# Optimization experiments

Measured on AMD Instinct MI355X. Metric: run time of the kernel, lower is better.

## Reference

```python
import jax, jax.numpy as jnp
import numpy as np

B, T, E, H = 4, 4096, 1024, 64

def setup_inputs() -> dict:
    key = jax.random.key(0)
    kx, kk, kq, kv = jax.random.split(key, 4)
    return {
        "x": jax.random.normal(kx, (B, T, E), dtype=jnp.float32),
        "Wk": jax.random.normal(kk, (E, H), dtype=jnp.float32) * (E ** -0.5),
        "Wq": jax.random.normal(kq, (E, H), dtype=jnp.float32) * (E ** -0.5),
        "Wv": jax.random.normal(kv, (E, H), dtype=jnp.float32) * (E ** -0.5),
    }

def reference(x, Wk, Wq, Wv):
    # x: [B, T, E]; projections: [B, T, H]
    k = jnp.einsum("bte,eh->bth", x, Wk)
    q = jnp.einsum("bte,eh->bth", x, Wq)
    v = jnp.einsum("bte,eh->bth", x, Wv)
    # NOTE: original scales by embedding dim (x.shape[-1]), not head dim.
    scale = x.shape[-1] ** -0.5
    scores = jnp.einsum("bqh,bkh->bqk", q, k) * scale  # [B, T, T]
    t = x.shape[1]
    causal = jnp.tril(jnp.ones((t, t), dtype=bool))
    scores = jnp.where(causal[None, :, :], scores, -jnp.inf)
    attn = jax.nn.softmax(scores, axis=-1)
    # dropout_rate = 0 (eval) -> identity
    return jnp.einsum("bqk,bkh->bqh", attn, v)
```

## Files before the change

kernel.cpp:

```cpp
#include <hip/hip_runtime.h>
#include <hip/hip_bf16.h>

typedef __attribute__((ext_vector_type(8))) short s16x8;
typedef __attribute__((ext_vector_type(4))) float f32x4;

#define TSEQ 4096
#define SPLIT 8

static __device__ __forceinline__ ushort f2bf(float f) {
    union { float f; unsigned u; } v; v.f = f;
    unsigned u = v.u;
    unsigned r = (u + 0x7fffu + ((u >> 16) & 1u)) >> 16;
    return (ushort)r;
}

static __device__ __forceinline__ s16x8 mk8(unsigned a, unsigned b, unsigned c, unsigned d) {
    union { uint4 u; s16x8 v; } x; x.u = make_uint4(a, b, c, d); return x.v;
}

static __device__ __forceinline__ void gload_lds16(const void* g, void* l) {
    __builtin_amdgcn_global_load_lds(
        (const __attribute__((address_space(1))) unsigned int*)g,
        (__attribute__((address_space(3))) unsigned int*)l, 16, 0, 0);
}

__global__ __launch_bounds__(256) void prep_w(const float* __restrict__ Wk,
                                              const float* __restrict__ Wq,
                                              const float* __restrict__ Wv,
                                              ushort* __restrict__ wt) {
    __shared__ float tile[64][65];
    int bid = blockIdx.x;
    int mi = bid >> 4;
    int e0 = (bid & 15) << 6;
    const float* src = (mi == 0) ? Wq : (mi == 1) ? Wk : Wv;
    int n = threadIdx.x & 63;
    int quad = threadIdx.x >> 6;
#pragma unroll
    for (int r = 0; r < 16; ++r) {
        int el = r * 4 + quad;
        tile[el][n] = src[(size_t)(e0 + el) * 64 + n];
    }
    __syncthreads();
    float scale = (mi == 0) ? 0.03125f : 1.0f;
    int ecol = threadIdx.x & 63;
#pragma unroll
    for (int r = 0; r < 16; ++r) {
        int nl = r * 4 + quad;
        wt[(size_t)(mi * 64 + nl) * 1024 + e0 + ecol] = f2bf(tile[ecol][nl] * scale);
    }
}

__global__ __launch_bounds__(512) void proj(const float* __restrict__ x,
                                            const ushort* __restrict__ wt,
                                            ushort* __restrict__ qb,
                                            ushort* __restrict__ kb,
                                            ushort* __restrict__ vt) {
    __shared__ char smem[3 * 40960];
    int tid = threadIdx.x;
    int lane = tid & 63, w = tid >> 6;
    int l15 = lane & 15, g = lane >> 4;
    int mh = w >> 2, nq = w & 3;
    size_t m0 = (size_t)blockIdx.x * 64;

    int rA = tid >> 4, sA = tid & 15;
    const float* xsrc = x + (m0 + rA) * 1024 + ((sA ^ (rA & 15)) << 2);
    int rB = tid >> 3, sB = tid & 7;
    const ushort* wsrc = wt + (size_t)rB * 1024 + ((sB ^ (rB & 7)) << 3);

    f32x4 acc[2][3];
#pragma unroll
    for (int mi = 0; mi < 2; ++mi)
#pragma unroll
        for (int j = 0; j < 3; ++j) acc[mi][j] = (f32x4){0.f, 0.f, 0.f, 0.f};

#define PSTAGE(bufsel, it) do {                                        \
        size_t k0_ = (size_t)(it) << 6;                                \
        char* bb_ = smem + (bufsel) * 40960;                           \
        gload_lds16(xsrc + k0_, bb_ + tid * 16);                       \
        gload_lds16(xsrc + 32 * 1024 + k0_, bb_ + 8192 + tid * 16);    \
        gload_lds16(wsrc + k0_, bb_ + 16384 + tid * 16);               \
        gload_lds16(wsrc + 64 * 1024 + k0_, bb_ + 24576 + tid * 16);   \
        gload_lds16(wsrc + 128 * 1024 + k0_, bb_ + 32768 + tid * 16);  \
    } while (0)

    PSTAGE(0, 0);
    PSTAGE(1, 1);
    for (int i = 0; i < 16; ++i) {
        int cur = i % 3;
        __builtin_amdgcn_sched_barrier(0);
        if (i < 15) asm volatile("s_waitcnt vmcnt(5)" ::: "memory");
        else        asm volatile("s_waitcnt vmcnt(0)" ::: "memory");
        __builtin_amdgcn_s_barrier();
        __builtin_amdgcn_sched_barrier(0);
        if (i + 2 < 16) PSTAGE((i + 2) % 3, i + 2);

        const char* Ab = smem + cur * 40960;
        const char* Bb = Ab + 16384;
#pragma unroll
        for (int ks = 0; ks < 2; ++ks) {
            s16x8 a[2];
#pragma unroll
            for (int mi = 0; mi < 2; ++mi) {
                int row = mh * 32 + mi * 16 + l15;
                int s0 = ks * 8 + g * 2;
                f32x4 xa = *(const f32x4*)(Ab + row * 256 + ((s0 ^ l15) << 4));
                f32x4 xb2 = *(const f32x4*)(Ab + row * 256 + (((s0 + 1) ^ l15) << 4));
#pragma unroll
                for (int q2 = 0; q2 < 4; ++q2) {
                    a[mi][q2] = (short)f2bf(xa[q2]);
                    a[mi][q2 + 4] = (short)f2bf(xb2[q2]);
                }
            }
#pragma unroll
            for (int j = 0; j < 3; ++j) {
                int n = nq * 48 + j * 16 + l15;
                s16x8 bf = *(const s16x8*)(Bb + n * 128 + (((ks * 4 + g) ^ (l15 & 7)) << 4));
#pragma unroll
                for (int mi = 0; mi < 2; ++mi)
                    acc[mi][j] = __builtin_amdgcn_mfma_f32_16x16x32_bf16(a[mi], bf, acc[mi][j], 0, 0, 0);
            }
        }
    }
#undef PSTAGE

    size_t bb = m0 >> 12;
    size_t t00 = m0 & 4095;
#pragma unroll
    for (int mi = 0; mi < 2; ++mi) {
        size_t Mb = m0 + mh * 32 + mi * 16 + 4 * g;
#pragma unroll
        for (int j = 0; j < 3; ++j) {
            int nf = nq * 3 + j;
            int n = nf * 16 + l15;
            if (nf < 4) {
#pragma unroll
                for (int r = 0; r < 4; ++r)
                    qb[(Mb + r) * 64 + n] = f2bf(acc[mi][j][r]);
            } else if (nf < 8) {
#pragma unroll
                for (int r = 0; r < 4; ++r)
                    kb[(Mb + r) * 64 + (n - 64)] = f2bf(acc[mi][j][r]);
            } else {
                int h = n - 128;
                size_t tloc = t00 + mh * 32 + mi * 16 + 4 * g;
                unsigned w0 = (unsigned)f2bf(acc[mi][j][0]) | ((unsigned)f2bf(acc[mi][j][1]) << 16);
                unsigned w1 = (unsigned)f2bf(acc[mi][j][2]) | ((unsigned)f2bf(acc[mi][j][3]) << 16);
                *(uint2*)(vt + (bb * 64 + h) * TSEQ + tloc) = make_uint2(w0, w1);
            }
        }
    }
}

__global__ __launch_bounds__(512) void attn(const ushort* __restrict__ qb,
                                            const ushort* __restrict__ kb,
                                            const ushort* __restrict__ vt,
                                            float* __restrict__ po,
                                            float2* __restrict__ pml) {
    __shared__ char smem[34816];
    int tid = threadIdx.x;
    int lane = tid & 63, w = tid >> 6;
    int l15 = lane & 15, g = lane >> 4;
    int bid = blockIdx.x;
    int s = bid & 7;
    int b = (bid >> 3) & 3;
    int idx = bid >> 5;
    int p = (idx < 16) ? (31 - idx) : (idx - 16);
    int q0w = p * 128 + w * 16;
    int q = q0w + l15;
    int my_tmax = q0w >> 6;
    int nkvb = 2 * p + 2;
    int cnt = (s < nkvb) ? ((nkvb + 7 - s) >> 3) : 0;

    int row = tid >> 3;
    int kswz = (((tid & 7) ^ (row & 7)) << 3);

    const ushort* qbase = qb + ((size_t)b * TSEQ + q) * 64;
    s16x8 qf0 = *(const s16x8*)(qbase + g * 8);
    s16x8 qf1 = *(const s16x8*)(qbase + 32 + g * 8);

    f32x4 o[4];
#pragma unroll
    for (int i = 0; i < 4; ++i) o[i] = (f32x4){0.f, 0.f, 0.f, 0.f};
    float m = -1e30f, lsum = 0.f;

#define STAGE(bufsel, tt) do {                                                         \
        const ushort* ksrc_ = kb + ((size_t)b * TSEQ + (size_t)(tt) * 64 + row) * 64 + kswz; \
        gload_lds16(ksrc_, smem + (bufsel) * 8192 + tid * 16);                         \
        const ushort* vsrc_ = vt + ((size_t)b * 64 + row) * TSEQ + (size_t)(tt) * 64 + kswz; \
        gload_lds16(vsrc_, smem + 16384 + (bufsel) * 8192 + tid * 16);                 \
    } while (0)

    if (cnt > 0) {
        STAGE(0, s);
        asm volatile("s_waitcnt vmcnt(0)" ::: "memory");
        __builtin_amdgcn_s_barrier();
        __builtin_amdgcn_sched_barrier(0);
        for (int i = 0; i < cnt; ++i) {
            int t = s + (i << 3);
            int cur = i & 1;
            if (i + 1 < cnt) STAGE(cur ^ 1, t + 8);
            if (t <= my_tmax) {
                const char* Kb = smem + cur * 8192;
                const char* Vb = smem + 16384 + cur * 8192;
                int swz = (l15 & 7) << 4;

                f32x4 st[4];
#pragma unroll
                for (int kf = 0; kf < 4; ++kf) {
                    const char* kr = Kb + (kf * 16 + l15) * 128;
                    s16x8 ka0 = *(const s16x8*)(kr + ((g * 16) ^ swz));
                    s16x8 ka1 = *(const s16x8*)(kr + ((64 + g * 16) ^ swz));
                    f32x4 z = (f32x4){0.f, 0.f, 0.f, 0.f};
                    z = __builtin_amdgcn_mfma_f32_16x16x32_bf16(ka0, qf0, z, 0, 0, 0);
                    st[kf] = __builtin_amdgcn_mfma_f32_16x16x32_bf16(ka1, qf1, z, 0, 0, 0);
                }

                if (t == my_tmax) {
#pragma unroll
                    for (int kf = 0; kf < 4; ++kf) {
#pragma unroll
                        for (int r = 0; r < 4; ++r) {
                            int k = (t << 6) + kf * 16 + 4 * g + r;
                            if (k > q) st[kf][r] = -1e30f;
                        }
                    }
                }

                float pmax = st[0][0];
#pragma unroll
                for (int kf = 0; kf < 4; ++kf) {
#pragma unroll
                    for (int r = 0; r < 4; ++r) pmax = fmaxf(pmax, st[kf][r]);
                }
                pmax = fmaxf(pmax, __shfl_xor(pmax, 16, 64));
                pmax = fmaxf(pmax, __shfl_xor(pmax, 32, 64));
                float mnew = fmaxf(m, pmax);
                float sf = __expf(m - mnew);
                m = mnew;

                float psum = 0.f;
                ushort pb[4][4];
#pragma unroll
                for (int kf = 0; kf < 4; ++kf) {
#pragma unroll
                    for (int r = 0; r < 4; ++r) {
                        float pv = __expf(st[kf][r] - mnew);
                        psum += pv;
                        pb[kf][r] = f2bf(pv);
                    }
                }
                lsum = lsum * sf + psum;
#pragma unroll
                for (int i2 = 0; i2 < 4; ++i2) {
                    o[i2][0] *= sf; o[i2][1] *= sf; o[i2][2] *= sf; o[i2][3] *= sf;
                }

                unsigned pw[4][2];
#pragma unroll
                for (int kf = 0; kf < 4; ++kf) {
                    pw[kf][0] = (unsigned)pb[kf][0] | ((unsigned)pb[kf][1] << 16);
                    pw[kf][1] = (unsigned)pb[kf][2] | ((unsigned)pb[kf][3] << 16);
                }
#pragma unroll
                for (int ks = 0; ks < 2; ++ks) {
                    s16x8 pf = mk8(pw[2 * ks][0], pw[2 * ks][1], pw[2 * ks + 1][0], pw[2 * ks + 1][1]);
#pragma unroll
                    for (int hf = 0; hf < 4; ++hf) {
                        const char* vr = Vb + (hf * 16 + l15) * 128;
                        uint2 lo = *(const uint2*)(vr + ((ks * 64 + g * 8) ^ swz));
                        uint2 hi = *(const uint2*)(vr + ((ks * 64 + 32 + g * 8) ^ swz));
                        o[hf] = __builtin_amdgcn_mfma_f32_16x16x32_bf16(
                            mk8(lo.x, lo.y, hi.x, hi.y), pf, o[hf], 0, 0, 0);
                    }
                }
            }
            __builtin_amdgcn_sched_barrier(0);
            asm volatile("s_waitcnt vmcnt(0)" ::: "memory");
            __builtin_amdgcn_s_barrier();
            __builtin_amdgcn_sched_barrier(0);
        }
    }
#undef STAGE

    __syncthreads();

    lsum += __shfl_xor(lsum, 16, 64);
    lsum += __shfl_xor(lsum, 32, 64);

    float* ot = (float*)(smem + w * 4352);
#pragma unroll
    for (int hf = 0; hf < 4; ++hf) {
#pragma unroll
        for (int r = 0; r < 4; ++r)
            ot[l15 * 68 + hf * 16 + 4 * g + r] = o[hf][r];
    }
    int rowq = lane >> 2, quad = lane & 3;
    size_t obase = ((size_t)s * 16384 + b * 4096 + q0w + rowq) * 64 + quad * 16;
#pragma unroll
    for (int j = 0; j < 4; ++j) {
        f32x4 vv = *(const f32x4*)&ot[rowq * 68 + quad * 16 + j * 4];
        *(f32x4*)(po + obase + j * 4) = vv;
    }
    if (lane < 16) {
        pml[(size_t)s * 16384 + b * 4096 + q0w + l15] = make_float2(m, lsum);
    }
}

__global__ __launch_bounds__(256) void merge(const float* __restrict__ po,
                                             const float2* __restrict__ pml,
                                             float* __restrict__ out) {
    int gt = blockIdx.x * 256 + threadIdx.x;
    int rowq = gt >> 4;
    int h4 = (gt & 15) << 2;
    float ms[SPLIT], ls[SPLIT];
    float M = -1e30f;
#pragma unroll
    for (int s2 = 0; s2 < SPLIT; ++s2) {
        float2 ml = pml[(size_t)s2 * 16384 + rowq];
        ms[s2] = ml.x; ls[s2] = ml.y;
        M = fmaxf(M, ml.x);
    }
    float L = 0.f;
    float ww[SPLIT];
#pragma unroll
    for (int s2 = 0; s2 < SPLIT; ++s2) {
        float e = __expf(ms[s2] - M);
        ww[s2] = e;
        L += ls[s2] * e;
    }
    f32x4 acc = (f32x4){0.f, 0.f, 0.f, 0.f};
#pragma unroll
    for (int s2 = 0; s2 < SPLIT; ++s2) {
        f32x4 v = *(const f32x4*)(po + ((size_t)s2 * 16384 + rowq) * 64 + h4);
        acc += v * ww[s2];
    }
    float inv = 1.0f / L;
    *(f32x4*)(out + (size_t)rowq * 64 + h4) = acc * inv;
}

extern "C" void kernel_launch(void* const* d_in, const int* in_sizes, int n_in,
                              void* d_out, int out_size, void* d_ws, size_t ws_size,
                              hipStream_t stream) {
    (void)in_sizes; (void)n_in; (void)out_size; (void)ws_size;
    const float* x  = (const float*)d_in[0];
    const float* Wk = (const float*)d_in[1];
    const float* Wq = (const float*)d_in[2];
    const float* Wv = (const float*)d_in[3];
    float* out = (float*)d_out;

    char* ws = (char*)d_ws;
    ushort* wt = (ushort*)(ws);
    ushort* qb = (ushort*)(ws + (1u << 20));
    ushort* kb = (ushort*)(ws + (3u << 20));
    ushort* vt = (ushort*)(ws + (5u << 20));
    float*  po = (float*)(ws + ((size_t)8 << 20));
    float2* pml = (float2*)(ws + ((size_t)40 << 20));

    prep_w<<<48, 256, 0, stream>>>(Wk, Wq, Wv, wt);
    proj<<<256, 512, 0, stream>>>(x, wt, qb, kb, vt);
    attn<<<1024, 512, 0, stream>>>(qb, kb, vt, po, pml);
    merge<<<1024, 256, 0, stream>>>(po, pml, out);
}
```

Baseline: 142.2 us.

## Triple-buffer KV loads, use exp2 with lazy rescale, store bf16 partials

The attention loop moves from double to triple buffering of K/V tiles in LDS. It waits with vmcnt(2) so two tiles are in flight, and drops the trailing barrier. The q pre-scale now folds in log2(e) so raw v_exp_f32 (exp2) replaces __expf. The online-softmax rescale of o and lsum is skipped unless some lane's max grows by more than 8, which trims exp and multiply work. Partial outputs are written as bf16 instead of fp32, halving the traffic between attn and merge, at some accuracy cost.

```diff
diff --git a/kernel.cpp b/kernel.cpp
--- a/kernel.cpp
+++ b/kernel.cpp
@@ -12,6 +12,14 @@
     unsigned u = v.u;
     unsigned r = (u + 0x7fffu + ((u >> 16) & 1u)) >> 16;
     return (ushort)r;
+}
+
+static __device__ __forceinline__ float bf2f(unsigned lo16) {
+    union { unsigned u; float f; } v; v.u = lo16 << 16; return v.f;
+}
+
+static __device__ __forceinline__ float fexp2(float x) {
+    float r; asm("v_exp_f32 %0, %1" : "=v"(r) : "v"(x)); return r;
 }
 
 static __device__ __forceinline__ s16x8 mk8(unsigned a, unsigned b, unsigned c, unsigned d) {
@@ -41,7 +49,7 @@
         tile[el][n] = src[(size_t)(e0 + el) * 64 + n];
     }
     __syncthreads();
-    float scale = (mi == 0) ? 0.03125f : 1.0f;
+    float scale = (mi == 0) ? 0.045084224f : 1.0f;
     int ecol = threadIdx.x & 63;
 #pragma unroll
     for (int r = 0; r < 16; ++r) {
@@ -154,9 +162,9 @@
 __global__ __launch_bounds__(512) void attn(const ushort* __restrict__ qb,
                                             const ushort* __restrict__ kb,
                                             const ushort* __restrict__ vt,
-                                            float* __restrict__ po,
+                                            ushort* __restrict__ po,
                                             float2* __restrict__ pml) {
-    __shared__ char smem[34816];
+    __shared__ char smem[49152];
     int tid = threadIdx.x;
     int lane = tid & 63, w = tid >> 6;
     int l15 = lane & 15, g = lane >> 4;
@@ -187,21 +195,25 @@
         const ushort* ksrc_ = kb + ((size_t)b * TSEQ + (size_t)(tt) * 64 + row) * 64 + kswz; \
         gload_lds16(ksrc_, smem + (bufsel) * 8192 + tid * 16);                         \
         const ushort* vsrc_ = vt + ((size_t)b * 64 + row) * TSEQ + (size_t)(tt) * 64 + kswz; \
-        gload_lds16(vsrc_, smem + 16384 + (bufsel) * 8192 + tid * 16);                 \
+        gload_lds16(vsrc_, smem + 24576 + (bufsel) * 8192 + tid * 16);                 \
     } while (0)
 
     if (cnt > 0) {
         STAGE(0, s);
-        asm volatile("s_waitcnt vmcnt(0)" ::: "memory");
-        __builtin_amdgcn_s_barrier();
-        __builtin_amdgcn_sched_barrier(0);
+        if (cnt > 1) STAGE(1, s + 8);
         for (int i = 0; i < cnt; ++i) {
             int t = s + (i << 3);
-            int cur = i & 1;
-            if (i + 1 < cnt) STAGE(cur ^ 1, t + 8);
+            int cur = i % 3;
+            __builtin_amdgcn_sched_barrier(0);
+            if (i + 1 < cnt) asm volatile("s_waitcnt vmcnt(2)" ::: "memory");
+            else             asm volatile("s_waitcnt vmcnt(0)" ::: "memory");
+            __builtin_amdgcn_s_barrier();
+            __builtin_amdgcn_sched_barrier(0);
+            if (i + 2 < cnt) STAGE((i + 2) % 3, t + 16);
+
             if (t <= my_tmax) {
                 const char* Kb = smem + cur * 8192;
-                const char* Vb = smem + 16384 + cur * 8192;
+                const char* Vb = smem + 24576 + cur * 8192;
                 int swz = (l15 & 7) << 4;
 
                 f32x4 st[4];
@@ -234,9 +246,17 @@
                 }
                 pmax = fmaxf(pmax, __shfl_xor(pmax, 16, 64));
                 pmax = fmaxf(pmax, __shfl_xor(pmax, 32, 64));
-                float mnew = fmaxf(m, pmax);
-                float sf = __expf(m - mnew);
-                m = mnew;
+
+                if (!__all(pmax - m <= 8.0f)) {
+                    float mnew = fmaxf(m, pmax);
+                    float sf = fexp2(m - mnew);
+                    m = mnew;
+                    lsum *= sf;
+#pragma unroll
+                    for (int i2 = 0; i2 < 4; ++i2) {
+                        o[i2][0] *= sf; o[i2][1] *= sf; o[i2][2] *= sf; o[i2][3] *= sf;
+                    }
+                }
 
                 float psum = 0.f;
                 ushort pb[4][4];
@@ -244,16 +264,12 @@
                 for (int kf = 0; kf < 4; ++kf) {
 #pragma unroll
                     for (int r = 0; r < 4; ++r) {
-                        float pv = __expf(st[kf][r] - mnew);
+                        float pv = fexp2(st[kf][r] - m);
                         psum += pv;
                         pb[kf][r] = f2bf(pv);
                     }
                 }
-                lsum = lsum * sf + psum;
-#pragma unroll
-                for (int i2 = 0; i2 < 4; ++i2) {
-                    o[i2][0] *= sf; o[i2][1] *= sf; o[i2][2] *= sf; o[i2][3] *= sf;
-                }
+                lsum += psum;
 
                 unsigned pw[4][2];
 #pragma unroll
@@ -274,10 +290,6 @@
                     }
                 }
             }
-            __builtin_amdgcn_sched_barrier(0);
-            asm volatile("s_waitcnt vmcnt(0)" ::: "memory");
-            __builtin_amdgcn_s_barrier();
-            __builtin_amdgcn_sched_barrier(0);
         }
     }
 #undef STAGE
@@ -295,18 +307,21 @@
             ot[l15 * 68 + hf * 16 + 4 * g + r] = o[hf][r];
     }
     int rowq = lane >> 2, quad = lane & 3;
-    size_t obase = ((size_t)s * 16384 + b * 4096 + q0w + rowq) * 64 + quad * 16;
-#pragma unroll
-    for (int j = 0; j < 4; ++j) {
-        f32x4 vv = *(const f32x4*)&ot[rowq * 68 + quad * 16 + j * 4];
-        *(f32x4*)(po + obase + j * 4) = vv;
-    }
+    const float* src = &ot[rowq * 68 + quad * 16];
+    unsigned pk[8];
+#pragma unroll
+    for (int j = 0; j < 8; ++j)
+        pk[j] = (unsigned)f2bf(src[2 * j]) | ((unsigned)f2bf(src[2 * j + 1]) << 16);
+    ushort* dst = po + ((size_t)s * 16384 + b * 4096 + q0w + rowq) * 64 + quad * 16;
+    *(uint4*)dst = make_uint4(pk[0], pk[1], pk[2], pk[3]);
+    *(uint4*)(dst + 8) = make_uint4(pk[4], pk[5], pk[6], pk[7]);
+
     if (lane < 16) {
         pml[(size_t)s * 16384 + b * 4096 + q0w + l15] = make_float2(m, lsum);
     }
 }
 
-__global__ __launch_bounds__(256) void merge(const float* __restrict__ po,
+__global__ __launch_bounds__(256) void merge(const ushort* __restrict__ po,
                                              const float2* __restrict__ pml,
                                              float* __restrict__ out) {
     int gt = blockIdx.x * 256 + threadIdx.x;
@@ -324,15 +339,19 @@
     float ww[SPLIT];
 #pragma unroll
     for (int s2 = 0; s2 < SPLIT; ++s2) {
-        float e = __expf(ms[s2] - M);
+        float e = fexp2(ms[s2] - M);
         ww[s2] = e;
         L += ls[s2] * e;
     }
     f32x4 acc = (f32x4){0.f, 0.f, 0.f, 0.f};
 #pragma unroll
     for (int s2 = 0; s2 < SPLIT; ++s2) {
-        f32x4 v = *(const f32x4*)(po + ((size_t)s2 * 16384 + rowq) * 64 + h4);
-        acc += v * ww[s2];
+        uint2 pv = *(const uint2*)(po + ((size_t)s2 * 16384 + rowq) * 64 + h4);
+        float wgt = ww[s2];
+        acc[0] += wgt * bf2f(pv.x & 0xffffu);
+        acc[1] += wgt * bf2f(pv.x >> 16);
+        acc[2] += wgt * bf2f(pv.y & 0xffffu);
+        acc[3] += wgt * bf2f(pv.y >> 16);
     }
     float inv = 1.0f / L;
     *(f32x4*)(out + (size_t)rowq * 64 + h4) = acc * inv;
@@ -353,8 +372,8 @@
     ushort* qb = (ushort*)(ws + (1u << 20));
     ushort* kb = (ushort*)(ws + (3u << 20));
     ushort* vt = (ushort*)(ws + (5u << 20));
-    float*  po = (float*)(ws + ((size_t)8 << 20));
-    float2* pml = (float2*)(ws + ((size_t)40 << 20));
+    ushort* po = (ushort*)(ws + ((size_t)8 << 20));
+    float2* pml = (float2*)(ws + ((size_t)26 << 20));
 
     prep_w<<<48, 256, 0, stream>>>(Wk, Wq, Wv, wt);
     proj<<<256, 512, 0, stream>>>(x, wt, qb, kb, vt);
```

Measured after the change: 139.4 us. 1.02x faster.
